# Kernel tuning notes

Hardware: AMD Instinct MI355X
Metric: run time of the kernel (lower is better)

The kernel has to match this reference:

```python
import jax, jax.numpy as jnp
import numpy as np

N_HEADS = 16

def setup_inputs() -> dict:
    key = jax.random.key(0)
    k1, k2 = jax.random.split(key)
    B, S, H = 4, 2048, 1024
    hidden_states = jax.random.normal(k1, (B, S, H), dtype=jnp.float32)
    # F.linear weight: [out_features, in_features]; init std per module
    std = 0.02 / np.sqrt(2.0 * 24 * H)
    queries_weight = jax.random.normal(k2, (H, H), dtype=jnp.float32) * std
    return {"hidden_states": hidden_states, "queries_weight": queries_weight}


def reference(hidden_states, queries_weight):
    B, S, H = hidden_states.shape
    hd = H // N_HEADS
    # F.linear: x @ W^T
    q = hidden_states @ queries_weight.T
    qh = q.reshape(B, S, N_HEADS, hd)          # [B,S,h,d]
    xh = hidden_states.reshape(B, S, N_HEADS, hd)
    # pre_attn = Q K^T (no softmax), then attn @ V with K=V=x heads
    pre_attn = jnp.einsum('bqhd,bkhd->bhqk', qh, xh)   # [B,h,S,S]
    attn = jnp.einsum('bhqk,bkhd->bqhd', pre_attn, xh) # [B,S,h,d]
    return attn.reshape(B, S, H)
```

## Files before the change

### kernel.cpp

```cpp
#include <hip/hip_runtime.h>
#include <hip/hip_bf16.h>


typedef __bf16 bf16x8 __attribute__((ext_vector_type(8)));
typedef float f32x4 __attribute__((ext_vector_type(4)));

typedef __attribute__((address_space(3))) unsigned int lds_u32;
typedef const __attribute__((address_space(1))) unsigned int glb_u32;

__device__ __forceinline__ void gld_lds16(const void* g, void* l) {
    __builtin_amdgcn_global_load_lds((glb_u32*)g, (lds_u32*)l, 16, 0, 0);
}

__device__ __forceinline__ unsigned short f2bf(float f) {
    unsigned int u = __float_as_uint(f);
    u += 0x7FFFu + ((u >> 16) & 1u);
    return (unsigned short)(u >> 16);
}

__global__ __launch_bounds__(256) void gx_partial(
        const float* __restrict__ x, const float* __restrict__ W,
        unsigned short* __restrict__ xb, unsigned short* __restrict__ Wb,
        float* __restrict__ Gp) {
    __shared__ __align__(16) unsigned short xt[2][64 * 128];
    const int tid = threadIdx.x;
    const int chunk = blockIdx.x;
    const int bh = blockIdx.y;
    const int fb = bh * 8 + chunk;
    const int b = bh >> 4, h = bh & 15;
    const int wave = tid >> 6, lane = tid & 63;
    const int lm = lane & 15, quad = lane >> 4;

    {
        size_t base = (size_t)fb * 2048 + (size_t)tid * 8;
        float4 v0 = *(const float4*)&W[base];
        float4 v1 = *(const float4*)&W[base + 4];
        ushort4 o0 = {f2bf(v0.x), f2bf(v0.y), f2bf(v0.z), f2bf(v0.w)};
        ushort4 o1 = {f2bf(v1.x), f2bf(v1.y), f2bf(v1.z), f2bf(v1.w)};
        *(ushort4*)&Wb[base] = o0;
        *(ushort4*)&Wb[base + 4] = o1;
    }

    const int sc = (tid & 15) * 4;
    const int sr = tid >> 4;
    const size_t gcol = (size_t)h * 64 + sc;
    const int wsz0 = ((tid & 7) ^ 0) << 3;
    const int wsz1 = ((tid & 7) ^ 2) << 3;
    const int wsz2 = ((tid & 7) ^ 4) << 3;
    const int wsz3 = ((tid & 7) ^ 6) << 3;
    const int rA = wave * 16 + lm;
    const int swzA = ((((rA >> 2) & 7) ^ ((rA & 3) << 1)) << 3);
    int swzB[4];
    #pragma unroll
    for (int ni = 0; ni < 4; ++ni) {
        int rb = ni * 16 + lm;
        swzB[ni] = ((((rb >> 2) & 7) ^ ((rb & 3) << 1)) << 3);
    }
    const int colq = quad * 8;
    const size_t row0 = (size_t)(b * 2048 + chunk * 256);

    f32x4 acc[4] = {};
    float4 v[8];

    #pragma unroll
    for (int i = 0; i < 8; ++i)
        v[i] = *(const float4*)&x[(row0 + sr + 16 * i) * 1024 + gcol];
    #pragma unroll
    for (int i = 0; i < 8; ++i) {
        int s = sr + 16 * i;
        ushort4 o = {f2bf(v[i].x), f2bf(v[i].y), f2bf(v[i].z), f2bf(v[i].w)};
        *(ushort4*)&xb[(row0 + s) * 1024 + gcol] = o;
        xt[0][(sc + 0) * 128 + (s ^ wsz0)] = o.x;
        xt[0][(sc + 1) * 128 + (s ^ wsz1)] = o.y;
        xt[0][(sc + 2) * 128 + (s ^ wsz2)] = o.z;
        xt[0][(sc + 3) * 128 + (s ^ wsz3)] = o.w;
    }
    __syncthreads();

    #pragma unroll
    for (int i = 0; i < 8; ++i)
        v[i] = *(const float4*)&x[(row0 + 128 + sr + 16 * i) * 1024 + gcol];

    #pragma unroll
    for (int k = 0; k < 4; ++k) {
        bf16x8 af = *(const bf16x8*)&xt[0][rA * 128 + ((k * 32 + colq) ^ swzA)];
        #pragma unroll
        for (int ni = 0; ni < 4; ++ni) {
            bf16x8 bg = *(const bf16x8*)&xt[0][(ni * 16 + lm) * 128 + ((k * 32 + colq) ^ swzB[ni])];
            acc[ni] = __builtin_amdgcn_mfma_f32_16x16x32_bf16(af, bg, acc[ni], 0, 0, 0);
        }
    }

    #pragma unroll
    for (int i = 0; i < 8; ++i) {
        int s = sr + 16 * i;
        ushort4 o = {f2bf(v[i].x), f2bf(v[i].y), f2bf(v[i].z), f2bf(v[i].w)};
        *(ushort4*)&xb[(row0 + 128 + s) * 1024 + gcol] = o;
        xt[1][(sc + 0) * 128 + (s ^ wsz0)] = o.x;
        xt[1][(sc + 1) * 128 + (s ^ wsz1)] = o.y;
        xt[1][(sc + 2) * 128 + (s ^ wsz2)] = o.z;
        xt[1][(sc + 3) * 128 + (s ^ wsz3)] = o.w;
    }
    __syncthreads();

    #pragma unroll
    for (int k = 0; k < 4; ++k) {
        bf16x8 af = *(const bf16x8*)&xt[1][rA * 128 + ((k * 32 + colq) ^ swzA)];
        #pragma unroll
        for (int ni = 0; ni < 4; ++ni) {
            bf16x8 bg = *(const bf16x8*)&xt[1][(ni * 16 + lm) * 128 + ((k * 32 + colq) ^ swzB[ni])];
            acc[ni] = __builtin_amdgcn_mfma_f32_16x16x32_bf16(af, bg, acc[ni], 0, 0, 0);
        }
    }

    float* gp = Gp + ((size_t)(chunk * 64 + bh)) * 4096;
    #pragma unroll
    for (int ni = 0; ni < 4; ++ni)
        #pragma unroll
        for (int r = 0; r < 4; ++r)
            gp[(wave * 16 + quad * 4 + r) * 64 + ni * 16 + lm] = acc[ni][r];
}

__global__ __launch_bounds__(256) void g_reduce(
        const float* __restrict__ Gp, unsigned short* __restrict__ Gb) {
    const int bh = blockIdx.x;
    const int e0 = blockIdx.y * 1024 + threadIdx.x * 4;
    float4 s = {0.f, 0.f, 0.f, 0.f};
    #pragma unroll
    for (int c = 0; c < 8; ++c) {
        float4 v = *(const float4*)&Gp[((size_t)(c * 64 + bh)) * 4096 + e0];
        s.x += v.x; s.y += v.y; s.z += v.z; s.w += v.w;
    }
    ushort4 o;
    o.x = f2bf(s.x); o.y = f2bf(s.y); o.z = f2bf(s.z); o.w = f2bf(s.w);
    *(ushort4*)&Gb[(size_t)bh * 4096 + e0] = o;
}

__global__ __launch_bounds__(256, 2) void gemm_qout(
        const unsigned short* __restrict__ xb, const unsigned short* __restrict__ Wb,
        const unsigned short* __restrict__ Gb, float* __restrict__ out) {
    __shared__ __align__(16) unsigned short smem[32768];
    unsigned short* lA0 = smem;
    unsigned short* lB0 = smem + 8192;
    unsigned short* lA1 = smem + 16384;
    unsigned short* lB1 = smem + 24576;
    unsigned short* Qt  = smem;
    unsigned short* G2  = smem + 17408;
    const int tid = threadIdx.x;
    const int m0 = blockIdx.x * 128;
    const int n0 = blockIdx.y * 128;
    const int b  = blockIdx.x >> 4;
    const int h0 = blockIdx.y * 2;
    const int lane = tid & 63, wave = tid >> 6;
    const int wr = (wave >> 1) * 64, wc = (wave & 1) * 64;
    const int lm = lane & 15, quad = lane >> 4;
    const int srow = wave * 32 + (lane >> 3);
    const int scol = (((lane & 7) ^ ((lane >> 3) & 7))) * 8;

    uint4 gr[4];
    #pragma unroll
    for (int i = 0; i < 4; ++i) {
        int idx = tid + 256 * i;
        int hh = idx >> 9;
        int rr = (idx >> 3) & 63;
        int cc = (idx & 7) * 8;
        gr[i] = *(const uint4*)&Gb[((size_t)(b * 16 + h0 + hh)) * 4096 + rr * 64 + cc];
    }

    const unsigned short* gaBase = &xb[(size_t)(m0 + srow) * 1024 + scol];
    const unsigned short* gbBase = &Wb[(size_t)(n0 + srow) * 1024 + scol];

#define STAGE(pA, pB, KT)                                                     \
    {                                                                         \
        _Pragma("unroll")                                                     \
        for (int i = 0; i < 4; ++i) {                                         \
            gld_lds16(gaBase + (KT) + (size_t)i * 8 * 1024,                   \
                      &(pA)[(wave * 32 + i * 8) * 64]);                       \
            gld_lds16(gbBase + (KT) + (size_t)i * 8 * 1024,                   \
                      &(pB)[(wave * 32 + i * 8) * 64]);                       \
        }                                                                     \
    }

#define COMPUTE(pA, pB)                                                       \
    {                                                                         \
        _Pragma("unroll")                                                     \
        for (int kk = 0; kk < 2; ++kk) {                                      \
            bf16x8 af[4], bg[4];                                              \
            _Pragma("unroll")                                                 \
            for (int mi = 0; mi < 4; ++mi) {                                  \
                int ra = wr + mi * 16 + lm;                                   \
                int jb = (kk * 4 + quad) ^ (ra & 7);                          \
                af[mi] = *(const bf16x8*)&(pA)[ra * 64 + jb * 8];             \
            }                                                                 \
            _Pragma("unroll")                                                 \
            for (int ni = 0; ni < 4; ++ni) {                                  \
                int rb = wc + ni * 16 + lm;                                   \
                int jb = (kk * 4 + quad) ^ (rb & 7);                          \
                bg[ni] = *(const bf16x8*)&(pB)[rb * 64 + jb * 8];             \
            }                                                                 \
            _Pragma("unroll")                                                 \
            for (int mi = 0; mi < 4; ++mi)                                    \
                _Pragma("unroll")                                             \
                for (int ni = 0; ni < 4; ++ni)                                \
                    acc[mi][ni] = __builtin_amdgcn_mfma_f32_16x16x32_bf16(    \
                        af[mi], bg[ni], acc[mi][ni], 0, 0, 0);                \
        }                                                                     \
    }

    f32x4 acc[4][4] = {};
    STAGE(lA0, lB0, 0);
    __syncthreads();
    for (int kt = 0; kt < 1024; kt += 128) {
        STAGE(lA1, lB1, kt + 64);
        COMPUTE(lA0, lB0);
        __syncthreads();
        if (kt + 128 < 1024) STAGE(lA0, lB0, kt + 128);
        COMPUTE(lA1, lB1);
        __syncthreads();
    }
#undef STAGE
#undef COMPUTE

    #pragma unroll
    for (int mi = 0; mi < 4; ++mi)
        #pragma unroll
        for (int ni = 0; ni < 4; ++ni)
            #pragma unroll
            for (int r = 0; r < 4; ++r)
                Qt[(wr + mi * 16 + quad * 4 + r) * 136 + wc + ni * 16 + lm] =
                    f2bf(acc[mi][ni][r]);
    #pragma unroll
    for (int i = 0; i < 4; ++i) {
        int idx = tid + 256 * i;
        int hh = idx >> 9;
        int rr = (idx >> 3) & 63;
        int cc = (idx & 7) * 8;
        *(uint4*)&G2[hh * 4608 + rr * 72 + cc] = gr[i];
    }
    __syncthreads();
    #pragma unroll
    for (int mi = 0; mi < 4; ++mi)
        #pragma unroll
        for (int ni = 0; ni < 4; ++ni)
            acc[mi][ni] = (f32x4){0.f, 0.f, 0.f, 0.f};
    const int hh = wave & 1;
    #pragma unroll
    for (int kk = 0; kk < 2; ++kk) {
        bf16x8 af[4], bg[4];
        #pragma unroll
        for (int mi = 0; mi < 4; ++mi)
            af[mi] = *(const bf16x8*)&Qt[(wr + mi * 16 + lm) * 136 + wc + kk * 32 + quad * 8];
        #pragma unroll
        for (int ni = 0; ni < 4; ++ni)
            bg[ni] = *(const bf16x8*)&G2[hh * 4608 + (ni * 16 + lm) * 72 + kk * 32 + quad * 8];
        #pragma unroll
        for (int mi = 0; mi < 4; ++mi)
            #pragma unroll
            for (int ni = 0; ni < 4; ++ni)
                acc[mi][ni] = __builtin_amdgcn_mfma_f32_16x16x32_bf16(
                    af[mi], bg[ni], acc[mi][ni], 0, 0, 0);
    }
    #pragma unroll
    for (int mi = 0; mi < 4; ++mi)
        #pragma unroll
        for (int ni = 0; ni < 4; ++ni)
            #pragma unroll
            for (int r = 0; r < 4; ++r)
                out[(size_t)(m0 + wr + mi * 16 + quad * 4 + r) * 1024
                    + n0 + wc + ni * 16 + lm] = acc[mi][ni][r];
}

extern "C" void kernel_launch(void* const* d_in, const int* in_sizes, int n_in,
                              void* d_out, int out_size, void* d_ws, size_t ws_size,
                              hipStream_t stream) {
    const float* x = (const float*)d_in[0];
    const float* W = (const float*)d_in[1];
    float* out = (float*)d_out;
    char* ws = (char*)d_ws;
    unsigned short* xb = (unsigned short*)(ws);
    unsigned short* Wb = (unsigned short*)(ws + 16777216);
    float*          Gp = (float*)        (ws + 18874368);
    unsigned short* Gb = (unsigned short*)(ws + 27262976);

    gx_partial<<<dim3(8, 64), 256, 0, stream>>>(x, W, xb, Wb, Gp);
    g_reduce<<<dim3(64, 4), 256, 0, stream>>>(Gp, Gb);
    gemm_qout<<<dim3(64, 8), 256, 0, stream>>>(xb, Wb, Gb, out);
}
```

Baseline: 122.4 us.

## Enlarge gemm_qout tile to 256x128 with 8 waves and triple-buffered LDS pipeline

```diff
diff --git a/kernel.cpp b/kernel.cpp
--- a/kernel.cpp
+++ b/kernel.cpp
@@ -136,49 +136,42 @@
     *(ushort4*)&Gb[(size_t)bh * 4096 + e0] = o;
 }
 
-__global__ __launch_bounds__(256, 2) void gemm_qout(
+__global__ __launch_bounds__(512, 1) void gemm_qout(
         const unsigned short* __restrict__ xb, const unsigned short* __restrict__ Wb,
         const unsigned short* __restrict__ Gb, float* __restrict__ out) {
-    __shared__ __align__(16) unsigned short smem[32768];
-    unsigned short* lA0 = smem;
-    unsigned short* lB0 = smem + 8192;
-    unsigned short* lA1 = smem + 16384;
-    unsigned short* lB1 = smem + 24576;
-    unsigned short* Qt  = smem;
-    unsigned short* G2  = smem + 17408;
+    extern __shared__ __align__(16) unsigned short smem[];
     const int tid = threadIdx.x;
-    const int m0 = blockIdx.x * 128;
+    const int m0 = blockIdx.x * 256;
     const int n0 = blockIdx.y * 128;
-    const int b  = blockIdx.x >> 4;
+    const int b  = blockIdx.x >> 3;
     const int h0 = blockIdx.y * 2;
     const int lane = tid & 63, wave = tid >> 6;
-    const int wr = (wave >> 1) * 64, wc = (wave & 1) * 64;
+    const int wr = (wave >> 1) * 64;
+    const int wc = (wave & 1) * 64;
     const int lm = lane & 15, quad = lane >> 4;
-    const int srow = wave * 32 + (lane >> 3);
-    const int scol = (((lane & 7) ^ ((lane >> 3) & 7))) * 8;
-
-    uint4 gr[4];
-    #pragma unroll
-    for (int i = 0; i < 4; ++i) {
-        int idx = tid + 256 * i;
-        int hh = idx >> 9;
-        int rr = (idx >> 3) & 63;
-        int cc = (idx & 7) * 8;
-        gr[i] = *(const uint4*)&Gb[((size_t)(b * 16 + h0 + hh)) * 4096 + rr * 64 + cc];
-    }
-
-    const unsigned short* gaBase = &xb[(size_t)(m0 + srow) * 1024 + scol];
-    const unsigned short* gbBase = &Wb[(size_t)(n0 + srow) * 1024 + scol];
+    const int srow8 = lane >> 3;
+    const int scol = (((lane & 7) ^ (srow8 & 7))) * 8;
+
+    const unsigned short* gaBase = &xb[(size_t)(m0 + wave * 32 + srow8) * 1024 + scol];
+    const unsigned short* gbBase = &Wb[(size_t)(n0 + wave * 16 + srow8) * 1024 + scol];
+
+    unsigned short* A0 = smem;
+    unsigned short* B0 = smem + 16384;
+    unsigned short* A1 = smem + 24576;
+    unsigned short* B1 = smem + 40960;
+    unsigned short* A2 = smem + 49152;
+    unsigned short* B2 = smem + 65536;
 
 #define STAGE(pA, pB, KT)                                                     \
     {                                                                         \
         _Pragma("unroll")                                                     \
-        for (int i = 0; i < 4; ++i) {                                         \
+        for (int i = 0; i < 4; ++i)                                           \
             gld_lds16(gaBase + (KT) + (size_t)i * 8 * 1024,                   \
                       &(pA)[(wave * 32 + i * 8) * 64]);                       \
+        _Pragma("unroll")                                                     \
+        for (int i = 0; i < 2; ++i)                                           \
             gld_lds16(gbBase + (KT) + (size_t)i * 8 * 1024,                   \
-                      &(pB)[(wave * 32 + i * 8) * 64]);                       \
-        }                                                                     \
+                      &(pB)[(wave * 16 + i * 8) * 64]);                       \
     }
 
 #define COMPUTE(pA, pB)                                                       \
@@ -208,19 +201,31 @@
     }
 
     f32x4 acc[4][4] = {};
-    STAGE(lA0, lB0, 0);
-    __syncthreads();
-    for (int kt = 0; kt < 1024; kt += 128) {
-        STAGE(lA1, lB1, kt + 64);
-        COMPUTE(lA0, lB0);
-        __syncthreads();
-        if (kt + 128 < 1024) STAGE(lA0, lB0, kt + 128);
-        COMPUTE(lA1, lB1);
-        __syncthreads();
+    STAGE(A0, B0, 0);
+    STAGE(A1, B1, 64);
+    for (int t = 0; t < 16; ++t) {
+        if (t < 14) {
+            STAGE(A2, B2, (t + 2) * 64);
+            asm volatile("s_waitcnt vmcnt(12)" ::: "memory");
+        } else if (t == 14) {
+            asm volatile("s_waitcnt vmcnt(6)" ::: "memory");
+        } else {
+            asm volatile("s_waitcnt vmcnt(0)" ::: "memory");
+        }
+        __builtin_amdgcn_sched_barrier(0);
+        asm volatile("s_barrier" ::: "memory");
+        __builtin_amdgcn_s_setprio(1);
+        COMPUTE(A0, B0);
+        __builtin_amdgcn_s_setprio(0);
+        asm volatile("s_barrier" ::: "memory");
+        unsigned short* tA = A0; A0 = A1; A1 = A2; A2 = tA;
+        unsigned short* tB = B0; B0 = B1; B1 = B2; B2 = tB;
     }
 #undef STAGE
 #undef COMPUTE
 
+    unsigned short* Qt = smem;
+    unsigned short* G2 = smem + 34816;
     #pragma unroll
     for (int mi = 0; mi < 4; ++mi)
         #pragma unroll
@@ -230,14 +235,15 @@
                 Qt[(wr + mi * 16 + quad * 4 + r) * 136 + wc + ni * 16 + lm] =
                     f2bf(acc[mi][ni][r]);
     #pragma unroll
-    for (int i = 0; i < 4; ++i) {
-        int idx = tid + 256 * i;
+    for (int i = 0; i < 2; ++i) {
+        int idx = tid + 512 * i;
         int hh = idx >> 9;
         int rr = (idx >> 3) & 63;
         int cc = (idx & 7) * 8;
-        *(uint4*)&G2[hh * 4608 + rr * 72 + cc] = gr[i];
-    }
-    __syncthreads();
+        *(uint4*)&G2[hh * 4608 + rr * 72 + cc] =
+            *(const uint4*)&Gb[((size_t)(b * 16 + h0 + hh)) * 4096 + rr * 64 + cc];
+    }
+    asm volatile("s_barrier" ::: "memory");
     #pragma unroll
     for (int mi = 0; mi < 4; ++mi)
         #pragma unroll
@@ -284,5 +290,5 @@
 
     gx_partial<<<dim3(8, 64), 256, 0, stream>>>(x, W, xb, Wb, Gp);
     g_reduce<<<dim3(64, 4), 256, 0, stream>>>(Gp, Gb);
-    gemm_qout<<<dim3(64, 8), 256, 0, stream>>>(xb, Wb, Gb, out);
-}
+    gemm_qout<<<dim3(32, 8), 512, 147456, stream>>>(xb, Wb, Gb, out);
+}
```

Result: faster. 114.9 us (-6.2%).
